# Optimization experiments

Hardware: AMD Instinct MI355X
Metric: run time of the kernel (lower is better)

Reference implementation:

```python
import jax, jax.numpy as jnp
import numpy as np

B, K, C = 512, 64, 2048  # batch, mixture components, copy (eval points)


def setup_inputs() -> dict:
    key = jax.random.key(0)
    kw, km, ks, kr, kx = jax.random.split(key, 5)
    w = jax.random.uniform(kw, (B, K), dtype=jnp.float32)            # mixture weights
    means = jax.random.normal(km, (B, K, 2), dtype=jnp.float32)      # mean1, mean2
    sds = jax.random.uniform(ks, (B, K, 2), dtype=jnp.float32,
                             minval=0.5, maxval=1.5)                 # sd1, sd2 (>0)
    corr = jax.random.uniform(kr, (B, K), dtype=jnp.float32,
                              minval=-0.8, maxval=0.8)               # |corr| < 1
    model_out = jnp.concatenate(
        [w[..., None], means, sds, corr[..., None]], axis=-1)        # [B, K, 6]
    X = jax.random.normal(kx, (B, C, 2), dtype=jnp.float32)
    return {"model_out": model_out, "X": X}


def reference(model_out, X):
    # Unpack params: w, mean1, mean2, sd1, sd2, corr  -- each [B, K]
    w = model_out[..., 0]
    m1 = model_out[..., 1]
    m2 = model_out[..., 2]
    s1 = model_out[..., 3]
    s2 = model_out[..., 4]
    r = model_out[..., 5]

    # Closed-form bivariate normal pdf (equivalent to Cholesky-based
    # MultivariateNormal log_prob for the 2x2 covariance built in torch).
    # dx, dy: [B, C, K] via broadcasting X[B,C,1] against params[B,1,K]
    dx = (X[:, :, 0:1] - m1[:, None, :]) / s1[:, None, :]
    dy = (X[:, :, 1:2] - m2[:, None, :]) / s2[:, None, :]
    rb = r[:, None, :]
    omr2 = 1.0 - rb * rb  # 1 - rho^2
    z = dx * dx - 2.0 * rb * dx * dy + dy * dy
    two_pi = 2.0 * jnp.pi
    norm = two_pi * s1[:, None, :] * s2[:, None, :] * jnp.sqrt(omr2)
    probs = jnp.exp(-0.5 * z / omr2) / norm  # [B, C, K]

    # Weighted sum over components -> [B, C]
    return jnp.einsum('bck,bk->bc', probs, w)
```

## Files before the change

kernel.cpp:

```cpp
#include <hip/hip_runtime.h>


typedef float v2f __attribute__((ext_vector_type(2)));

constexpr int B = 512;
constexpr int K = 64;
constexpr int C = 2048;
constexpr int BLOCK = 256;
constexpr int HALVES = 2;
constexpr int CH = C / HALVES;

__device__ __forceinline__ v2f splat(float v) { return (v2f){v, v}; }

__global__ __launch_bounds__(BLOCK, 4) void mixture_kernel(
    const float* __restrict__ mo,
    const float* __restrict__ X,
    float* __restrict__ out)
{
    __shared__ float4 P[K][2];

    const int bid = blockIdx.x;
    const int b   = bid >> 1;
    const int h   = bid & 1;
    const int t   = threadIdx.x;

    if (t < K) {
        const float* p6 = mo + ((size_t)(b * K + t)) * 6;
        const float w  = p6[0];
        const float m1 = p6[1];
        const float m2 = p6[2];
        const float s1 = p6[3];
        const float s2 = p6[4];
        const float r  = p6[5];

        const float omr2 = fmaf(-r, r, 1.0f);
        const float inv  = 1.0f / omr2;
        const float g    = 0.7213475204444817f * inv;
        const float i1   = 1.0f / s1;
        const float i2   = 1.0f / s2;
        const float p    = g * i1 * i1;
        const float q    = g * i2 * i2;
        const float s    = 2.0f * r * g * i1 * i2;
        const float A    = -p;
        const float Bc   = -q;
        const float Cc   = s;
        const float D    = fmaf(2.0f * p, m1, -s * m2);
        const float E    = fmaf(2.0f * q, m2, -s * m1);
        const float wn   = w * 0.15915494309189535f * i1 * i2 * sqrtf(inv);
        const float L    = log2f(fmaxf(wn, 1e-37f));
        const float F    = fmaf(-p, m1 * m1, fmaf(-q, m2 * m2, fmaf(s, m1 * m2, L)));

        P[t][0] = make_float4(A, Bc, Cc, D);
        P[t][1] = make_float4(E, F, 0.0f, 0.0f);
    }
    __syncthreads();

    const float4* Xb = (const float4*)(X + (size_t)b * C * 2 + (size_t)h * CH * 2);
    const float4 xv0 = Xb[t];
    const float4 xv1 = Xb[t + BLOCK];

    const v2f xp[2]  = { {xv0.x, xv0.z}, {xv1.x, xv1.z} };
    const v2f yp[2]  = { {xv0.y, xv0.w}, {xv1.y, xv1.w} };
    const v2f xx[2]  = { xp[0] * xp[0], xp[1] * xp[1] };
    const v2f yy[2]  = { yp[0] * yp[0], yp[1] * yp[1] };
    const v2f xy[2]  = { xp[0] * yp[0], xp[1] * yp[1] };
    v2f acc[2] = { {0.0f, 0.0f}, {0.0f, 0.0f} };

#pragma unroll 4
    for (int k = 0; k < K; ++k) {
        const float4 c0 = P[k][0];
        const float4 c1 = P[k][1];
        const v2f A2 = splat(c0.x);
        const v2f B2 = splat(c0.y);
        const v2f C2 = splat(c0.z);
        const v2f D2 = splat(c0.w);
        const v2f E2 = splat(c1.x);
        const v2f F2 = splat(c1.y);

#pragma unroll
        for (int j = 0; j < 2; ++j) {
            v2f e = __builtin_elementwise_fma(A2, xx[j], F2);
            e     = __builtin_elementwise_fma(B2, yy[j], e);
            e     = __builtin_elementwise_fma(C2, xy[j], e);
            e     = __builtin_elementwise_fma(D2, xp[j], e);
            e     = __builtin_elementwise_fma(E2, yp[j], e);
            v2f ex;
            ex.x = __builtin_amdgcn_exp2f(e.x);
            ex.y = __builtin_amdgcn_exp2f(e.y);
            acc[j] = acc[j] + ex;
        }
    }

    float2* ob = (float2*)(out + (size_t)b * C + (size_t)h * CH);
    ob[t]         = make_float2(acc[0].x, acc[0].y);
    ob[t + BLOCK] = make_float2(acc[1].x, acc[1].y);
}

extern "C" void kernel_launch(void* const* d_in, const int* in_sizes, int n_in,
                              void* d_out, int out_size, void* d_ws, size_t ws_size,
                              hipStream_t stream) {
    const float* mo = (const float*)d_in[0];
    const float* X  = (const float*)d_in[1];
    float* out      = (float*)d_out;

    mixture_kernel<<<dim3(B * HALVES), dim3(BLOCK), 0, stream>>>(mo, X, out);
}
```

Baseline: 70.34 us.

## Split K across wave pairs with register-blocked points and LDS reduction

Each thread now handles 8 eval points (4 packed pairs) over half of the 64 components, with the two wave groups covering different K halves. Partial sums are combined through a shared-memory reduction buffer before a vectorized float4 store. Parameters are packed two components per 12 floats so each k-pair needs three float4 LDS loads, which raises ALU work per LDS parameter load. The cost is an extra barrier, 8KB more LDS per block, and higher register pressure from larger per-thread state.

```diff
diff --git a/kernel.cpp b/kernel.cpp
--- a/kernel.cpp
+++ b/kernel.cpp
@@ -9,20 +9,24 @@
 constexpr int BLOCK = 256;
 constexpr int HALVES = 2;
 constexpr int CH = C / HALVES;
-
-__device__ __forceinline__ v2f splat(float v) { return (v2f){v, v}; }
+constexpr int NP = 4;
 
 __global__ __launch_bounds__(BLOCK, 4) void mixture_kernel(
     const float* __restrict__ mo,
     const float* __restrict__ X,
     float* __restrict__ out)
 {
-    __shared__ float4 P[K][2];
+    __shared__ float  Pc[(K / 2) * 12];
+    __shared__ float  Rbuf[2][CH];
 
-    const int bid = blockIdx.x;
-    const int b   = bid >> 1;
-    const int h   = bid & 1;
-    const int t   = threadIdx.x;
+    const int bid  = blockIdx.x;
+    const int b    = bid >> 1;
+    const int h    = bid & 1;
+    const int t    = threadIdx.x;
+    const int lane = t & 63;
+    const int wid  = t >> 6;
+    const int kH   = wid & 1;
+    const int pH   = wid >> 1;
 
     if (t < K) {
         const float* p6 = mo + ((size_t)(b * K + t)) * 6;
@@ -50,50 +54,88 @@
         const float L    = log2f(fmaxf(wn, 1e-37f));
         const float F    = fmaf(-p, m1 * m1, fmaf(-q, m2 * m2, fmaf(s, m1 * m2, L)));
 
-        P[t][0] = make_float4(A, Bc, Cc, D);
-        P[t][1] = make_float4(E, F, 0.0f, 0.0f);
+        float* dst = &Pc[(t >> 1) * 12 + (t & 1) * 6];
+        dst[0] = A; dst[1] = Bc; dst[2] = Cc;
+        dst[3] = D; dst[4] = E;  dst[5] = F;
     }
     __syncthreads();
 
-    const float4* Xb = (const float4*)(X + (size_t)b * C * 2 + (size_t)h * CH * 2);
-    const float4 xv0 = Xb[t];
-    const float4 xv1 = Xb[t + BLOCK];
+    const float4* Xb = (const float4*)(X + ((size_t)b * C + (size_t)h * CH) * 2);
+    v2f xp[NP], yp[NP], xx[NP], yy[NP], xy[NP], acc[NP];
+#pragma unroll
+    for (int p = 0; p < NP; ++p) {
+        const float4 f4 = Xb[pH * 256 + p * 64 + lane];
+        xp[p]  = (v2f){f4.x, f4.z};
+        yp[p]  = (v2f){f4.y, f4.w};
+        xx[p]  = xp[p] * xp[p];
+        yy[p]  = yp[p] * yp[p];
+        xy[p]  = xp[p] * yp[p];
+        acc[p] = (v2f){0.0f, 0.0f};
+    }
 
-    const v2f xp[2]  = { {xv0.x, xv0.z}, {xv1.x, xv1.z} };
-    const v2f yp[2]  = { {xv0.y, xv0.w}, {xv1.y, xv1.w} };
-    const v2f xx[2]  = { xp[0] * xp[0], xp[1] * xp[1] };
-    const v2f yy[2]  = { yp[0] * yp[0], yp[1] * yp[1] };
-    const v2f xy[2]  = { xp[0] * yp[0], xp[1] * yp[1] };
-    v2f acc[2] = { {0.0f, 0.0f}, {0.0f, 0.0f} };
+    const float4* Pq = (const float4*)Pc;
 
 #pragma unroll 4
-    for (int k = 0; k < K; ++k) {
-        const float4 c0 = P[k][0];
-        const float4 c1 = P[k][1];
-        const v2f A2 = splat(c0.x);
-        const v2f B2 = splat(c0.y);
-        const v2f C2 = splat(c0.z);
-        const v2f D2 = splat(c0.w);
-        const v2f E2 = splat(c1.x);
-        const v2f F2 = splat(c1.y);
+    for (int pr = 0; pr < 16; ++pr) {
+        const int pb = (kH * 16 + pr) * 3;
+        const float4 q0 = Pq[pb + 0];
+        const float4 q1 = Pq[pb + 1];
+        const float4 q2 = Pq[pb + 2];
 
+        {
+            const v2f A2 = {q0.x, q0.x}, B2 = {q0.y, q0.y}, C2 = {q0.z, q0.z};
+            const v2f D2 = {q0.w, q0.w}, E2 = {q1.x, q1.x}, F2 = {q1.y, q1.y};
 #pragma unroll
-        for (int j = 0; j < 2; ++j) {
-            v2f e = __builtin_elementwise_fma(A2, xx[j], F2);
-            e     = __builtin_elementwise_fma(B2, yy[j], e);
-            e     = __builtin_elementwise_fma(C2, xy[j], e);
-            e     = __builtin_elementwise_fma(D2, xp[j], e);
-            e     = __builtin_elementwise_fma(E2, yp[j], e);
-            v2f ex;
-            ex.x = __builtin_amdgcn_exp2f(e.x);
-            ex.y = __builtin_amdgcn_exp2f(e.y);
-            acc[j] = acc[j] + ex;
+            for (int p = 0; p < NP; ++p) {
+                v2f e = __builtin_elementwise_fma(A2, xx[p], F2);
+                e     = __builtin_elementwise_fma(B2, yy[p], e);
+                e     = __builtin_elementwise_fma(C2, xy[p], e);
+                e     = __builtin_elementwise_fma(D2, xp[p], e);
+                e     = __builtin_elementwise_fma(E2, yp[p], e);
+                v2f ex;
+                ex.x = __builtin_amdgcn_exp2f(e.x);
+                ex.y = __builtin_amdgcn_exp2f(e.y);
+                acc[p] = acc[p] + ex;
+            }
+        }
+        {
+            const v2f A2 = {q1.z, q1.z}, B2 = {q1.w, q1.w}, C2 = {q2.x, q2.x};
+            const v2f D2 = {q2.y, q2.y}, E2 = {q2.z, q2.z}, F2 = {q2.w, q2.w};
+#pragma unroll
+            for (int p = 0; p < NP; ++p) {
+                v2f e = __builtin_elementwise_fma(A2, xx[p], F2);
+                e     = __builtin_elementwise_fma(B2, yy[p], e);
+                e     = __builtin_elementwise_fma(C2, xy[p], e);
+                e     = __builtin_elementwise_fma(D2, xp[p], e);
+                e     = __builtin_elementwise_fma(E2, yp[p], e);
+                v2f ex;
+                ex.x = __builtin_amdgcn_exp2f(e.x);
+                ex.y = __builtin_amdgcn_exp2f(e.y);
+                acc[p] = acc[p] + ex;
+            }
         }
     }
 
-    float2* ob = (float2*)(out + (size_t)b * C + (size_t)h * CH);
-    ob[t]         = make_float2(acc[0].x, acc[0].y);
-    ob[t + BLOCK] = make_float2(acc[1].x, acc[1].y);
+    {
+        float2* rw = (float2*)&Rbuf[kH][pH * 512];
+#pragma unroll
+        for (int p = 0; p < NP; ++p)
+            rw[p * 64 + lane] = make_float2(acc[p].x, acc[p].y);
+    }
+    __syncthreads();
+
+    {
+        const float4* r0 = (const float4*)&Rbuf[0][0];
+        const float4* r1 = (const float4*)&Rbuf[1][0];
+        const float4 s0 = r0[t];
+        const float4 s1 = r1[t];
+        float4 s;
+        s.x = s0.x + s1.x;
+        s.y = s0.y + s1.y;
+        s.z = s0.z + s1.z;
+        s.w = s0.w + s1.w;
+        ((float4*)(out + (size_t)b * C + (size_t)h * CH))[t] = s;
+    }
 }
 
 extern "C" void kernel_launch(void* const* d_in, const int* in_sizes, int n_in,
```

After: 72.70 us. +3.4%, slower.
